# Kernel tuning notes

Measured on AMD Instinct MI355X. Metric: run time of the kernel, lower is better.

## Reference

```python
import jax, jax.numpy as jnp
import numpy as np

NEG = -1e9  # effectively -inf for masked logits, grad-safe

def apply_rope(t, cos, sin):
    # t: [b, H, S, D]; cos/sin: [S, D] -> rotate-half RoPE
    d = t.shape[-1]
    t1, t2 = t[..., : d // 2], t[..., d // 2 :]
    rot = jnp.concatenate([-t2, t1], axis=-1)
    return t * cos[None, None] + rot * sin[None, None]


def setup_inputs() -> dict:
    key = jax.random.key(0)
    ks = jax.random.split(key, 8)
    b, S, d_in = 1, 4096, 2048
    H, G, D = 16, 4, 128
    d_out = H * D
    sc = 1.0 / np.sqrt(d_in)
    x = jax.random.normal(ks[0], (b, S, d_in), dtype=jnp.float32)
    # causal mask: True = masked (future positions)
    mask = jnp.triu(jnp.ones((S, S), dtype=bool), k=1)
    inv = 1.0 / (10000.0 ** (jnp.arange(0, D, 2, dtype=jnp.float32) / D))
    ang = jnp.arange(S, dtype=jnp.float32)[:, None] * inv[None, :]  # [S, D/2]
    ang = jnp.concatenate([ang, ang], axis=-1)                      # [S, D]
    cos, sin = jnp.cos(ang), jnp.sin(ang)
    Wq = jax.random.normal(ks[1], (d_out, d_in), dtype=jnp.float32) * sc
    Wk = jax.random.normal(ks[2], (G * D, d_in), dtype=jnp.float32) * sc
    Wv = jax.random.normal(ks[3], (G * D, d_in), dtype=jnp.float32) * sc
    Wo = jax.random.normal(ks[4], (d_in, d_out), dtype=jnp.float32) * sc
    return {"x": x, "mask": mask, "cos": cos, "sin": sin,
            "Wq": Wq, "Wk": Wk, "Wv": Wv, "Wo": Wo}


def reference(x, mask, cos, sin, Wq, Wk, Wv, Wo):
    b, S, d_in = x.shape
    G = Wk.shape[0] // cos.shape[-1]          # num_kv_groups
    D = cos.shape[-1]                          # head_dim
    H = Wq.shape[0] // D                       # num_heads
    n = H // G                                 # group_size
    q = (x @ Wq.T).reshape(b, S, H, D).transpose(0, 2, 1, 3)   # [b,H,S,D]
    k = (x @ Wk.T).reshape(b, S, G, D).transpose(0, 2, 1, 3)   # [b,G,S,D]
    v = (x @ Wv.T).reshape(b, S, G, D).transpose(0, 2, 1, 3)
    q = apply_rope(q, cos, sin)
    k = apply_rope(k, cos, sin)
    # GQA: group heads instead of repeat_interleave (head h -> group h // n)
    qg = q.reshape(b, G, n, S, D)
    scores = jnp.einsum('bgnqd,bgkd->bgnqk', qg, k)            # [b,G,n,S,S]
    scores = jnp.where(mask[None, None, None], NEG, scores)
    w = jax.nn.softmax(scores / np.sqrt(D), axis=-1)
    ctx = jnp.einsum('bgnqk,bgkd->bgnqd', w, v)                # [b,G,n,S,D]
    ctx = ctx.reshape(b, H, S, D).transpose(0, 2, 1, 3).reshape(b, S, H * D)
    return ctx @ Wo.T
```

## Files before the change

kernel.cpp:

```cpp
#include <hip/hip_runtime.h>

typedef __attribute__((ext_vector_type(8))) short bf16x8;
typedef __attribute__((ext_vector_type(4))) short bf16x4;
typedef __attribute__((ext_vector_type(8))) unsigned short u16x8;
typedef __attribute__((ext_vector_type(4))) float f32x4;
typedef __attribute__((ext_vector_type(2))) unsigned int u32x2;

__device__ __forceinline__ unsigned short f2b(float f) {
  unsigned int u = __builtin_bit_cast(unsigned int, f);
  u += 0x7FFFu + ((u >> 16) & 1u);
  return (unsigned short)(u >> 16);
}
__device__ __forceinline__ float b2f(unsigned short h) {
  return __builtin_bit_cast(float, ((unsigned int)h) << 16);
}

__device__ __forceinline__ f32x4 mfma16x16x16(bf16x4 a, bf16x4 b, f32x4 c) {
#if __has_builtin(__builtin_amdgcn_mfma_f32_16x16x16bf16_1k)
  return __builtin_amdgcn_mfma_f32_16x16x16bf16_1k(a, b, c, 0, 0, 0);
#else
  asm volatile("v_mfma_f32_16x16x16_bf16 %0, %1, %2, %0" : "+v"(c) : "v"(a), "v"(b));
  return c;
#endif
}

__device__ __forceinline__ bf16x4 pack4(float a, float b, float c, float d) {
  unsigned int lo, hi;
  asm("v_cvt_pk_bf16_f32 %0, %1, %2" : "=v"(lo) : "v"(a), "v"(b));
  asm("v_cvt_pk_bf16_f32 %0, %1, %2" : "=v"(hi) : "v"(c), "v"(d));
  u32x2 u = {lo, hi};
  return __builtin_bit_cast(bf16x4, u);
}

#define AS1(p) (const __attribute__((address_space(1))) void*)(p)
#define AS3(p) (__attribute__((address_space(3))) void*)(p)

__device__ __forceinline__ void cvt8(const float* __restrict__ in,
                                     unsigned short* __restrict__ out,
                                     int i, float scale) {
  const float4* p = (const float4*)in + (size_t)i * 2;
  float4 a = p[0], b = p[1];
  u16x8 r;
  r[0] = f2b(a.x * scale); r[1] = f2b(a.y * scale);
  r[2] = f2b(a.z * scale); r[3] = f2b(a.w * scale);
  r[4] = f2b(b.x * scale); r[5] = f2b(b.y * scale);
  r[6] = f2b(b.z * scale); r[7] = f2b(b.w * scale);
  *((u16x8*)out + i) = r;
}

__global__ __launch_bounds__(256) void k_cvt_all(
    const float* __restrict__ x,  const float* __restrict__ Wq,
    const float* __restrict__ Wk, const float* __restrict__ Wv,
    const float* __restrict__ Wo, unsigned short* __restrict__ xb,
    unsigned short* __restrict__ wqkv, unsigned short* __restrict__ Wob,
    float sc) {
  int bid = blockIdx.x;
  int tid = threadIdx.x;
  if (bid < 4096)      cvt8(x,  xb,             (bid        ) * 256 + tid, 1.f);
  else if (bid < 6144) cvt8(Wq, wqkv,           (bid - 4096) * 256 + tid, sc);
  else if (bid < 6656) cvt8(Wk, wqkv + 4194304, (bid - 6144) * 256 + tid, 1.f);
  else if (bid < 7168) cvt8(Wv, wqkv + 5242880, (bid - 6656) * 256 + tid, 1.f);
  else                 cvt8(Wo, Wob,            (bid - 7168) * 256 + tid, 1.f);
}

__global__ __launch_bounds__(256) void k_post(unsigned short* __restrict__ qkv,
                                              const float* __restrict__ cosb,
                                              const float* __restrict__ sinb,
                                              unsigned short* __restrict__ vT) {
  __shared__ unsigned short tile[64][72];
  const int bid = blockIdx.x, t = threadIdx.x;
  if (bid < 2560) {
    int tid = bid * 256 + t;
    int oct = tid & 7;
    int hd  = (tid >> 3) % 20;
    int s   = (tid >> 3) / 20;
    unsigned short* p1 = qkv + (size_t)s * 3072 + hd * 128 + oct * 8;
    unsigned short* p2 = p1 + 64;
    u16x8 a = *(const u16x8*)p1;
    u16x8 b = *(const u16x8*)p2;
    const float4* cp = (const float4*)(cosb + (size_t)s * 128 + oct * 8);
    const float4* sp = (const float4*)(sinb + (size_t)s * 128 + oct * 8);
    float4 c0 = cp[0], c1 = cp[1], s0 = sp[0], s1 = sp[1];
    float cs[8] = {c0.x,c0.y,c0.z,c0.w,c1.x,c1.y,c1.z,c1.w};
    float sn[8] = {s0.x,s0.y,s0.z,s0.w,s1.x,s1.y,s1.z,s1.w};
    u16x8 ra, rb;
#pragma unroll
    for (int j = 0; j < 8; ++j) {
      float av = b2f(a[j]), bv = b2f(b[j]);
      ra[j] = f2b(av * cs[j] - bv * sn[j]);
      rb[j] = f2b(bv * cs[j] + av * sn[j]);
    }
    *(u16x8*)p1 = ra;
    *(u16x8*)p2 = rb;
  } else {
    int idx = bid - 2560;
    int bs = idx >> 3, bc = idx & 7;
#pragma unroll
    for (int i = 0; i < 2; ++i) {
      int c8 = t + 256 * i;
      int row = c8 >> 3, cb = c8 & 7;
      u16x8 v = *(const u16x8*)(qkv + (size_t)(bs * 64 + row) * 3072 + 2560 + bc * 64 + cb * 8);
#pragma unroll
      for (int j = 0; j < 8; ++j) tile[row][cb * 8 + j] = v[j];
    }
    __syncthreads();
#pragma unroll
    for (int i = 0; i < 2; ++i) {
      int c8 = t + 256 * i;
      int crow = c8 >> 3, sb = c8 & 7;
      u16x8 v;
#pragma unroll
      for (int j = 0; j < 8; ++j) v[j] = tile[sb * 8 + j][crow];
      *(u16x8*)(vT + (size_t)(bc * 64 + crow) * 4096 + bs * 64 + sb * 8) = v;
    }
  }
}

template <int OUTF32>
__global__ __launch_bounds__(256) void k_gemm_bt(
    const unsigned short* __restrict__ A, const unsigned short* __restrict__ B,
    void* __restrict__ C, int K, int lda, int ldb, int ldc) {
  __shared__ unsigned short As[128 * 64];
  __shared__ unsigned short Bs[128 * 64];
  const int t = threadIdx.x;
  const int lane = t & 63, w = t >> 6;
  const int wm = w >> 1, wn = w & 1;
  const int bn = blockIdx.x, bm = blockIdx.y;
  const unsigned short* Arow = A + (size_t)(bm * 128) * lda;
  const unsigned short* Brow = B + (size_t)(bn * 128) * ldb;

  f32x4 acc[4][4] = {};
  for (int kt = 0; kt < K; kt += 64) {
#pragma unroll
    for (int i = 0; i < 4; ++i) {
      int idx = i * 256 + t;
      int r = idx >> 3, blk = idx & 7;
      int sb = blk ^ (r & 7);
      __builtin_amdgcn_global_load_lds(AS1(Arow + (size_t)r * lda + kt + sb * 8),
                                       AS3(As + (i * 256 + w * 64) * 8), 16, 0, 0);
    }
#pragma unroll
    for (int i = 0; i < 4; ++i) {
      int idx = i * 256 + t;
      int r = idx >> 3, blk = idx & 7;
      int sb = blk ^ (r & 7);
      __builtin_amdgcn_global_load_lds(AS1(Brow + (size_t)r * ldb + kt + sb * 8),
                                       AS3(Bs + (i * 256 + w * 64) * 8), 16, 0, 0);
    }
    __syncthreads();
#pragma unroll
    for (int kk = 0; kk < 2; ++kk) {
      bf16x8 av[4], bv[4];
#pragma unroll
      for (int i = 0; i < 4; ++i) {
        int r = wm * 64 + i * 16 + (lane & 15);
        int off = (r * 128 + (kk * 32 + (lane >> 4) * 8) * 2) ^ ((r & 7) << 4);
        av[i] = *(const bf16x8*)((const char*)As + off);
      }
#pragma unroll
      for (int j = 0; j < 4; ++j) {
        int r = wn * 64 + j * 16 + (lane & 15);
        int off = (r * 128 + (kk * 32 + (lane >> 4) * 8) * 2) ^ ((r & 7) << 4);
        bv[j] = *(const bf16x8*)((const char*)Bs + off);
      }
#pragma unroll
      for (int i = 0; i < 4; ++i)
#pragma unroll
        for (int j = 0; j < 4; ++j)
          acc[i][j] = __builtin_amdgcn_mfma_f32_16x16x32_bf16(av[i], bv[j], acc[i][j], 0, 0, 0);
    }
    __syncthreads();
  }
#pragma unroll
  for (int i = 0; i < 4; ++i)
#pragma unroll
    for (int j = 0; j < 4; ++j)
#pragma unroll
      for (int r = 0; r < 4; ++r) {
        int m = bm * 128 + wm * 64 + i * 16 + (lane >> 4) * 4 + r;
        int n = bn * 128 + wn * 64 + j * 16 + (lane & 15);
        float v = acc[i][j][r];
        if (OUTF32) ((float*)C)[(size_t)m * ldc + n] = v;
        else        ((unsigned short*)C)[(size_t)m * ldc + n] = f2b(v);
      }
}

__global__ __launch_bounds__(256, 2) void k_attn(const unsigned short* __restrict__ qk,
                                                 const unsigned short* __restrict__ vT,
                                                 unsigned short* __restrict__ ctx) {
  __shared__ unsigned short Ks[2][64 * 128];
  __shared__ unsigned short Vs[2][64 * 128];
  const int b = blockIdx.x, h = blockIdx.y, g = h >> 2;
  const int t = threadIdx.x, lane = t & 63, w = t >> 6;
  const int l15 = lane & 15, lq = lane >> 4;
  const int xv = (l15 & 7) << 4;

  int kb[4], vb[4];
#pragma unroll
  for (int sl = 0; sl < 4; ++sl) kb[sl] = ((sl * 64 + lq * 16) ^ xv) + l15 * 256;
#pragma unroll
  for (int nt = 0; nt < 4; ++nt) vb[nt] = ((nt * 32 + lq * 8) ^ xv) + l15 * 128;

  const bf16x4 ones = { (short)0x3F80, (short)0x3F80, (short)0x3F80, (short)0x3F80 };

  for (int ph = 0; ph < 2; ++ph) {
    const int qt = ph ? 63 - b : b;
    const int qg = qt * 64 + w * 16 + l15;

    const unsigned short* kgp[4];
    const unsigned short* vgp[4];
    unsigned short* kld[4];
    unsigned short* vld[4];
#pragma unroll
    for (int i = 0; i < 4; ++i) {
      int idx = i * 256 + t;
      int r = idx >> 4, blk = idx & 15;
      int sb = (blk & 8) | ((blk ^ r) & 7);
      kgp[i] = qk + (size_t)r * 3072 + 2048 + g * 128 + sb * 8;
      kld[i] = (unsigned short*)Ks[0] + (size_t)(i * 256 + w * 64) * 8;
      int r2 = idx >> 3, blk2 = idx & 7;
      int sb2 = blk2 ^ (r2 & 7);
      vgp[i] = vT + (size_t)(g * 128 + r2) * 4096 + sb2 * 8;
      vld[i] = (unsigned short*)Vs[0] + (size_t)(i * 256 + w * 64) * 8;
    }

    bf16x8 aq[4];
    {
      const unsigned short* qb =
          qk + (size_t)(qt * 64 + w * 16 + l15) * 3072 + h * 128 + lq * 8;
#pragma unroll
      for (int sl = 0; sl < 4; ++sl) aq[sl] = *(const bf16x8*)(qb + sl * 32);
    }
    f32x4 o[8] = {};
    f32x4 osum = {};
    bf16x4 pa[4];

#pragma unroll
    for (int i = 0; i < 4; ++i) {
      __builtin_amdgcn_global_load_lds(AS1(kgp[i]), AS3(kld[i]), 16, 0, 0);
      __builtin_amdgcn_global_load_lds(AS1(vgp[i]), AS3(vld[i]), 16, 0, 0);
      kgp[i] += 64 * 3072;
      vgp[i] += 64;
    }
    asm volatile("s_waitcnt vmcnt(0)" ::: "memory");
    __builtin_amdgcn_s_barrier();

    for (int kt = 0; kt < qt; ++kt) {
      const int cur = kt & 1, nb = cur ^ 1;
      const char* Kc = (const char*)Ks[cur];
      const char* Vc = (const char*)Vs[cur];
#pragma unroll
      for (int i = 0; i < 4; ++i) {
        __builtin_amdgcn_global_load_lds(AS1(kgp[i]), AS3(kld[i] + nb * 8192), 16, 0, 0);
        __builtin_amdgcn_global_load_lds(AS1(vgp[i]), AS3(vld[i] + nb * 8192), 16, 0, 0);
        kgp[i] += 64 * 3072;
        vgp[i] += 64;
      }
      f32x4 st[4] = {};
      __builtin_amdgcn_s_setprio(1);
#pragma unroll
      for (int sl = 0; sl < 4; ++sl)
#pragma unroll
        for (int nt = 0; nt < 4; ++nt) {
          bf16x8 bk = *(const bf16x8*)(Kc + kb[sl] + nt * 4096);
          st[nt] = __builtin_amdgcn_mfma_f32_16x16x32_bf16(bk, aq[sl], st[nt], 0, 0, 0);
        }
      __builtin_amdgcn_s_setprio(0);
#pragma unroll
      for (int nt = 0; nt < 4; ++nt) {
        float p0 = __builtin_amdgcn_exp2f(st[nt][0]);
        float p1 = __builtin_amdgcn_exp2f(st[nt][1]);
        float p2 = __builtin_amdgcn_exp2f(st[nt][2]);
        float p3 = __builtin_amdgcn_exp2f(st[nt][3]);
        pa[nt] = pack4(p0, p1, p2, p3);
      }
      __builtin_amdgcn_s_setprio(1);
#pragma unroll
      for (int nt = 0; nt < 4; ++nt) {
        osum = mfma16x16x16(pa[nt], ones, osum);
#pragma unroll
        for (int dt = 0; dt < 8; ++dt) {
          bf16x4 vv = *(const bf16x4*)(Vc + vb[nt] + dt * 2048);
          o[dt] = mfma16x16x16(pa[nt], vv, o[dt]);
        }
      }
      __builtin_amdgcn_s_setprio(0);
      asm volatile("s_waitcnt vmcnt(0)" ::: "memory");
      __builtin_amdgcn_s_barrier();
    }
    {
      const char* Kc = (const char*)Ks[qt & 1];
      const char* Vc = (const char*)Vs[qt & 1];
      f32x4 st[4] = {};
      __builtin_amdgcn_s_setprio(1);
#pragma unroll
      for (int sl = 0; sl < 4; ++sl)
#pragma unroll
        for (int nt = 0; nt < 4; ++nt) {
          bf16x8 bk = *(const bf16x8*)(Kc + kb[sl] + nt * 4096);
          st[nt] = __builtin_amdgcn_mfma_f32_16x16x32_bf16(bk, aq[sl], st[nt], 0, 0, 0);
        }
      __builtin_amdgcn_s_setprio(0);
#pragma unroll
      for (int nt = 0; nt < 4; ++nt) {
        float pp[4];
#pragma unroll
        for (int r = 0; r < 4; ++r) {
          int key = qt * 64 + nt * 16 + lq * 4 + r;
          pp[r] = (key > qg) ? 0.f : __builtin_amdgcn_exp2f(st[nt][r]);
        }
        pa[nt] = pack4(pp[0], pp[1], pp[2], pp[3]);
      }
      __builtin_amdgcn_s_setprio(1);
#pragma unroll
      for (int nt = 0; nt < 4; ++nt) {
        osum = mfma16x16x16(pa[nt], ones, osum);
#pragma unroll
        for (int dt = 0; dt < 8; ++dt) {
          bf16x4 vv = *(const bf16x4*)(Vc + vb[nt] + dt * 2048);
          o[dt] = mfma16x16x16(pa[nt], vv, o[dt]);
        }
      }
      __builtin_amdgcn_s_setprio(0);
      __builtin_amdgcn_s_barrier();
    }

    float invq[4];
#pragma unroll
    for (int r = 0; r < 4; ++r) invq[r] = 1.f / osum[r];
#pragma unroll
    for (int dt = 0; dt < 8; ++dt)
#pragma unroll
      for (int r = 0; r < 4; ++r) {
        int q = qt * 64 + w * 16 + lq * 4 + r;
        int c = h * 128 + dt * 16 + l15;
        ctx[(size_t)q * 2048 + c] = f2b(o[dt][r] * invq[r]);
      }
  }
}

extern "C" void kernel_launch(void* const* d_in, const int* in_sizes, int n_in,
                              void* d_out, int out_size, void* d_ws, size_t ws_size,
                              hipStream_t stream) {
  const float* x    = (const float*)d_in[0];
  const float* cosb = (const float*)d_in[2];
  const float* sinb = (const float*)d_in[3];
  const float* Wq   = (const float*)d_in[4];
  const float* Wk   = (const float*)d_in[5];
  const float* Wv   = (const float*)d_in[6];
  const float* Wo   = (const float*)d_in[7];

  char* p = (char*)d_ws;
  unsigned short* xb   = (unsigned short*)p; p += (size_t)8388608 * 2;
  unsigned short* wqkv = (unsigned short*)p; p += (size_t)6291456 * 2;
  unsigned short* Wob  = (unsigned short*)p; p += (size_t)4194304 * 2;
  unsigned short* qkvb = (unsigned short*)p; p += (size_t)4096 * 3072 * 2;
  unsigned short* vTb  = (unsigned short*)p; p += (size_t)512 * 4096 * 2;
  unsigned short* ctx  = (unsigned short*)p; p += (size_t)4096 * 2048 * 2;
  if (ws_size < (size_t)(p - (char*)d_ws)) return;

  const float SC = 0.12751741f;

  k_cvt_all<<<9216, 256, 0, stream>>>(x, Wq, Wk, Wv, Wo, xb, wqkv, Wob, SC);

  k_gemm_bt<0><<<dim3(24, 32), 256, 0, stream>>>(xb, wqkv, qkvb, 2048, 2048, 2048, 3072);

  k_post<<<3072, 256, 0, stream>>>(qkvb, cosb, sinb, vTb);

  k_attn<<<dim3(32, 16), 256, 0, stream>>>(qkvb, vTb, ctx);

  k_gemm_bt<1><<<dim3(16, 32), 256, 0, stream>>>(ctx, Wob, d_out, 2048, 2048, 2048, 2048);
}
```

Baseline: 261.4 us.

## Process two GQA heads per attention block sharing K/V tiles, drop causal pairing

Each attention block now handles two query heads of the same KV group, so every K/V tile loaded into LDS feeds twice the MFMA work. This halves K/V global and LDS traffic per head. The grid changes from 32x16 blocks that each paired a short and a long query tile to 64x8 blocks with one query tile each, ordered longest-first. The cost is doubled accumulator registers, which may push past the register budget for two waves per SIMD. Dropping the balanced pairing also leaves per-block work uneven, relying on the reversed ordering to smooth the tail.

```diff
diff --git a/kernel.cpp b/kernel.cpp
--- a/kernel.cpp
+++ b/kernel.cpp
@@ -190,10 +190,13 @@
                                                  unsigned short* __restrict__ ctx) {
   __shared__ unsigned short Ks[2][64 * 128];
   __shared__ unsigned short Vs[2][64 * 128];
-  const int b = blockIdx.x, h = blockIdx.y, g = h >> 2;
+  const int qt = 63 - (int)blockIdx.x;
+  const int hp = blockIdx.y;
+  const int h0 = hp * 2, g = hp >> 1;
   const int t = threadIdx.x, lane = t & 63, w = t >> 6;
   const int l15 = lane & 15, lq = lane >> 4;
   const int xv = (l15 & 7) << 4;
+  const int qg = qt * 64 + w * 16 + l15;
 
   int kb[4], vb[4];
 #pragma unroll
@@ -203,140 +206,120 @@
 
   const bf16x4 ones = { (short)0x3F80, (short)0x3F80, (short)0x3F80, (short)0x3F80 };
 
-  for (int ph = 0; ph < 2; ++ph) {
-    const int qt = ph ? 63 - b : b;
-    const int qg = qt * 64 + w * 16 + l15;
-
-    const unsigned short* kgp[4];
-    const unsigned short* vgp[4];
-    unsigned short* kld[4];
-    unsigned short* vld[4];
+  const unsigned short* kgp[4];
+  const unsigned short* vgp[4];
+  unsigned short* kld[4];
+  unsigned short* vld[4];
+#pragma unroll
+  for (int i = 0; i < 4; ++i) {
+    int idx = i * 256 + t;
+    int r = idx >> 4, blk = idx & 15;
+    int sb = (blk & 8) | ((blk ^ r) & 7);
+    kgp[i] = qk + (size_t)r * 3072 + 2048 + g * 128 + sb * 8;
+    kld[i] = (unsigned short*)Ks[0] + (size_t)(i * 256 + w * 64) * 8;
+    int r2 = idx >> 3, blk2 = idx & 7;
+    int sb2 = blk2 ^ (r2 & 7);
+    vgp[i] = vT + (size_t)(g * 128 + r2) * 4096 + sb2 * 8;
+    vld[i] = (unsigned short*)Vs[0] + (size_t)(i * 256 + w * 64) * 8;
+  }
+
+  bf16x8 aq0[4], aq1[4];
+  {
+    const unsigned short* qb =
+        qk + (size_t)(qt * 64 + w * 16 + l15) * 3072 + h0 * 128 + lq * 8;
+#pragma unroll
+    for (int sl = 0; sl < 4; ++sl) {
+      aq0[sl] = *(const bf16x8*)(qb + sl * 32);
+      aq1[sl] = *(const bf16x8*)(qb + 128 + sl * 32);
+    }
+  }
+  f32x4 o0[8] = {}, o1[8] = {};
+  f32x4 osum0 = {}, osum1 = {};
+  bf16x4 pa0[4], pa1[4];
+
+#pragma unroll
+  for (int i = 0; i < 4; ++i) {
+    __builtin_amdgcn_global_load_lds(AS1(kgp[i]), AS3(kld[i]), 16, 0, 0);
+    __builtin_amdgcn_global_load_lds(AS1(vgp[i]), AS3(vld[i]), 16, 0, 0);
+    kgp[i] += 64 * 3072;
+    vgp[i] += 64;
+  }
+  asm volatile("s_waitcnt vmcnt(0)" ::: "memory");
+  __builtin_amdgcn_s_barrier();
+
+#define TILE(PAR, KT, MASKT)                                                   \
+  {                                                                            \
+    const char* Kc = (const char*)Ks[PAR];                                     \
+    const char* Vc = (const char*)Vs[PAR];                                     \
+    f32x4 st0[4] = {}, st1[4] = {};                                            \
+    __builtin_amdgcn_s_setprio(1);                                             \
+    _Pragma("unroll")                                                          \
+    for (int sl = 0; sl < 4; ++sl)                                             \
+      _Pragma("unroll")                                                        \
+      for (int nt = 0; nt < 4; ++nt) {                                         \
+        bf16x8 bk = *(const bf16x8*)(Kc + kb[sl] + nt * 4096);                 \
+        st0[nt] = __builtin_amdgcn_mfma_f32_16x16x32_bf16(bk, aq0[sl], st0[nt], 0, 0, 0); \
+        st1[nt] = __builtin_amdgcn_mfma_f32_16x16x32_bf16(bk, aq1[sl], st1[nt], 0, 0, 0); \
+      }                                                                        \
+    __builtin_amdgcn_s_setprio(0);                                             \
+    _Pragma("unroll")                                                          \
+    for (int nt = 0; nt < 4; ++nt) {                                           \
+      float q0[4], q1[4];                                                      \
+      _Pragma("unroll")                                                        \
+      for (int r = 0; r < 4; ++r) {                                            \
+        q0[r] = __builtin_amdgcn_exp2f(st0[nt][r]);                            \
+        q1[r] = __builtin_amdgcn_exp2f(st1[nt][r]);                            \
+        if (MASKT) {                                                           \
+          int key = (KT) * 64 + nt * 16 + lq * 4 + r;                          \
+          if (key > qg) { q0[r] = 0.f; q1[r] = 0.f; }                          \
+        }                                                                      \
+      }                                                                        \
+      pa0[nt] = pack4(q0[0], q0[1], q0[2], q0[3]);                             \
+      pa1[nt] = pack4(q1[0], q1[1], q1[2], q1[3]);                             \
+    }                                                                          \
+    __builtin_amdgcn_s_setprio(1);                                             \
+    _Pragma("unroll")                                                          \
+    for (int nt = 0; nt < 4; ++nt) {                                           \
+      osum0 = mfma16x16x16(pa0[nt], ones, osum0);                              \
+      osum1 = mfma16x16x16(pa1[nt], ones, osum1);                              \
+      _Pragma("unroll")                                                        \
+      for (int dt = 0; dt < 8; ++dt) {                                         \
+        bf16x4 vv = *(const bf16x4*)(Vc + vb[nt] + dt * 2048);                 \
+        o0[dt] = mfma16x16x16(pa0[nt], vv, o0[dt]);                            \
+        o1[dt] = mfma16x16x16(pa1[nt], vv, o1[dt]);                            \
+      }                                                                        \
+    }                                                                          \
+    __builtin_amdgcn_s_setprio(0);                                             \
+  }
+
+  for (int kt = 0; kt < qt; ++kt) {
+    const int cur = kt & 1, nb = cur ^ 1;
 #pragma unroll
     for (int i = 0; i < 4; ++i) {
-      int idx = i * 256 + t;
-      int r = idx >> 4, blk = idx & 15;
-      int sb = (blk & 8) | ((blk ^ r) & 7);
-      kgp[i] = qk + (size_t)r * 3072 + 2048 + g * 128 + sb * 8;
-      kld[i] = (unsigned short*)Ks[0] + (size_t)(i * 256 + w * 64) * 8;
-      int r2 = idx >> 3, blk2 = idx & 7;
-      int sb2 = blk2 ^ (r2 & 7);
-      vgp[i] = vT + (size_t)(g * 128 + r2) * 4096 + sb2 * 8;
-      vld[i] = (unsigned short*)Vs[0] + (size_t)(i * 256 + w * 64) * 8;
-    }
-
-    bf16x8 aq[4];
-    {
-      const unsigned short* qb =
-          qk + (size_t)(qt * 64 + w * 16 + l15) * 3072 + h * 128 + lq * 8;
-#pragma unroll
-      for (int sl = 0; sl < 4; ++sl) aq[sl] = *(const bf16x8*)(qb + sl * 32);
-    }
-    f32x4 o[8] = {};
-    f32x4 osum = {};
-    bf16x4 pa[4];
-
-#pragma unroll
-    for (int i = 0; i < 4; ++i) {
-      __builtin_amdgcn_global_load_lds(AS1(kgp[i]), AS3(kld[i]), 16, 0, 0);
-      __builtin_amdgcn_global_load_lds(AS1(vgp[i]), AS3(vld[i]), 16, 0, 0);
+      __builtin_amdgcn_global_load_lds(AS1(kgp[i]), AS3(kld[i] + nb * 8192), 16, 0, 0);
+      __builtin_amdgcn_global_load_lds(AS1(vgp[i]), AS3(vld[i] + nb * 8192), 16, 0, 0);
       kgp[i] += 64 * 3072;
       vgp[i] += 64;
     }
+    TILE(cur, kt, false)
     asm volatile("s_waitcnt vmcnt(0)" ::: "memory");
     __builtin_amdgcn_s_barrier();
-
-    for (int kt = 0; kt < qt; ++kt) {
-      const int cur = kt & 1, nb = cur ^ 1;
-      const char* Kc = (const char*)Ks[cur];
-      const char* Vc = (const char*)Vs[cur];
-#pragma unroll
-      for (int i = 0; i < 4; ++i) {
-        __builtin_amdgcn_global_load_lds(AS1(kgp[i]), AS3(kld[i] + nb * 8192), 16, 0, 0);
-        __builtin_amdgcn_global_load_lds(AS1(vgp[i]), AS3(vld[i] + nb * 8192), 16, 0, 0);
-        kgp[i] += 64 * 3072;
-        vgp[i] += 64;
-      }
-      f32x4 st[4] = {};
-      __builtin_amdgcn_s_setprio(1);
-#pragma unroll
-      for (int sl = 0; sl < 4; ++sl)
-#pragma unroll
-        for (int nt = 0; nt < 4; ++nt) {
-          bf16x8 bk = *(const bf16x8*)(Kc + kb[sl] + nt * 4096);
-          st[nt] = __builtin_amdgcn_mfma_f32_16x16x32_bf16(bk, aq[sl], st[nt], 0, 0, 0);
-        }
-      __builtin_amdgcn_s_setprio(0);
-#pragma unroll
-      for (int nt = 0; nt < 4; ++nt) {
-        float p0 = __builtin_amdgcn_exp2f(st[nt][0]);
-        float p1 = __builtin_amdgcn_exp2f(st[nt][1]);
-        float p2 = __builtin_amdgcn_exp2f(st[nt][2]);
-        float p3 = __builtin_amdgcn_exp2f(st[nt][3]);
-        pa[nt] = pack4(p0, p1, p2, p3);
-      }
-      __builtin_amdgcn_s_setprio(1);
-#pragma unroll
-      for (int nt = 0; nt < 4; ++nt) {
-        osum = mfma16x16x16(pa[nt], ones, osum);
-#pragma unroll
-        for (int dt = 0; dt < 8; ++dt) {
-          bf16x4 vv = *(const bf16x4*)(Vc + vb[nt] + dt * 2048);
-          o[dt] = mfma16x16x16(pa[nt], vv, o[dt]);
-        }
-      }
-      __builtin_amdgcn_s_setprio(0);
-      asm volatile("s_waitcnt vmcnt(0)" ::: "memory");
-      __builtin_amdgcn_s_barrier();
-    }
-    {
-      const char* Kc = (const char*)Ks[qt & 1];
-      const char* Vc = (const char*)Vs[qt & 1];
-      f32x4 st[4] = {};
-      __builtin_amdgcn_s_setprio(1);
-#pragma unroll
-      for (int sl = 0; sl < 4; ++sl)
-#pragma unroll
-        for (int nt = 0; nt < 4; ++nt) {
-          bf16x8 bk = *(const bf16x8*)(Kc + kb[sl] + nt * 4096);
-          st[nt] = __builtin_amdgcn_mfma_f32_16x16x32_bf16(bk, aq[sl], st[nt], 0, 0, 0);
-        }
-      __builtin_amdgcn_s_setprio(0);
-#pragma unroll
-      for (int nt = 0; nt < 4; ++nt) {
-        float pp[4];
-#pragma unroll
-        for (int r = 0; r < 4; ++r) {
-          int key = qt * 64 + nt * 16 + lq * 4 + r;
-          pp[r] = (key > qg) ? 0.f : __builtin_amdgcn_exp2f(st[nt][r]);
-        }
-        pa[nt] = pack4(pp[0], pp[1], pp[2], pp[3]);
-      }
-      __builtin_amdgcn_s_setprio(1);
-#pragma unroll
-      for (int nt = 0; nt < 4; ++nt) {
-        osum = mfma16x16x16(pa[nt], ones, osum);
-#pragma unroll
-        for (int dt = 0; dt < 8; ++dt) {
-          bf16x4 vv = *(const bf16x4*)(Vc + vb[nt] + dt * 2048);
-          o[dt] = mfma16x16x16(pa[nt], vv, o[dt]);
-        }
-      }
-      __builtin_amdgcn_s_setprio(0);
-      __builtin_amdgcn_s_barrier();
-    }
-
-    float invq[4];
-#pragma unroll
-    for (int r = 0; r < 4; ++r) invq[r] = 1.f / osum[r];
-#pragma unroll
-    for (int dt = 0; dt < 8; ++dt)
-#pragma unroll
-      for (int r = 0; r < 4; ++r) {
-        int q = qt * 64 + w * 16 + lq * 4 + r;
-        int c = h * 128 + dt * 16 + l15;
-        ctx[(size_t)q * 2048 + c] = f2b(o[dt][r] * invq[r]);
-      }
-  }
+  }
+  TILE(qt & 1, qt, true)
+#undef TILE
+
+  float iq0[4], iq1[4];
+#pragma unroll
+  for (int r = 0; r < 4; ++r) { iq0[r] = 1.f / osum0[r]; iq1[r] = 1.f / osum1[r]; }
+#pragma unroll
+  for (int dt = 0; dt < 8; ++dt)
+#pragma unroll
+    for (int r = 0; r < 4; ++r) {
+      int q = qt * 64 + w * 16 + lq * 4 + r;
+      int c = h0 * 128 + dt * 16 + l15;
+      ctx[(size_t)q * 2048 + c]       = f2b(o0[dt][r] * iq0[r]);
+      ctx[(size_t)q * 2048 + c + 128] = f2b(o1[dt][r] * iq1[r]);
+    }
 }
 
 extern "C" void kernel_launch(void* const* d_in, const int* in_sizes, int n_in,
@@ -367,7 +350,7 @@
 
   k_post<<<3072, 256, 0, stream>>>(qkvb, cosb, sinb, vTb);
 
-  k_attn<<<dim3(32, 16), 256, 0, stream>>>(qkvb, vTb, ctx);
+  k_attn<<<dim3(64, 8), 256, 0, stream>>>(qkvb, vTb, ctx);
 
   k_gemm_bt<1><<<dim3(16, 32), 256, 0, stream>>>(ctx, Wob, d_out, 2048, 2048, 2048, 2048);
 }
```

Measured after the change: 286.2 us. +9.5%, slower.
